# Kernel optimization log

Hardware: AMD Instinct MI355X
Metric: run time of the kernel (lower is better)

## Reference

```python
import jax, jax.numpy as jnp
import numpy as np

N_QUBITS = 4
N_LAYERS = 3
N_FEATURES = 64
BATCH = 524288


def setup_inputs() -> dict:
    key = jax.random.key(0)
    k1, k2, k3, k4 = jax.random.split(key, 4)
    x = jax.random.normal(k1, (BATCH, N_FEATURES), jnp.float32)
    # nn.Linear(64, 4) params
    lim = 1.0 / np.sqrt(N_FEATURES)
    W_pre = jax.random.uniform(k2, (N_QUBITS, N_FEATURES), jnp.float32, -lim, lim)
    b_pre = jax.random.uniform(k3, (N_QUBITS,), jnp.float32, -lim, lim)
    # quantum circuit weights: randn * 0.1
    qweights = jax.random.normal(k4, (N_LAYERS, N_QUBITS, 2), jnp.float32) * 0.1
    return {"x": x, "W_pre": W_pre, "b_pre": b_pre, "qweights": qweights}


def _coef(theta, n):
    # reshape scalar or [B] angle to broadcast against [B, 2,..,2] (n-1 trailing dims after slicing)
    return jnp.reshape(theta, (-1,) + (1,) * (n - 1))


def _apply_ry(state, wire, theta):
    # RY(t) = [[cos t/2, -sin t/2], [sin t/2, cos t/2]] applied on `wire`
    n = state.ndim - 1
    s = jnp.moveaxis(state, 1 + wire, -1)
    a, b = s[..., 0], s[..., 1]
    c = _coef(jnp.cos(theta / 2), n)
    sn = _coef(jnp.sin(theta / 2), n)
    out = jnp.stack([c * a - sn * b, sn * a + c * b], axis=-1)
    return jnp.moveaxis(out, -1, 1 + wire)


def _apply_rz(state, wire, theta):
    # RZ(t) = diag(e^{-i t/2}, e^{+i t/2})
    n = state.ndim - 1
    s = jnp.moveaxis(state, 1 + wire, -1)
    half = _coef(theta / 2, n)
    out = jnp.stack([jnp.exp(-1j * half) * s[..., 0],
                     jnp.exp(1j * half) * s[..., 1]], axis=-1)
    return jnp.moveaxis(out, -1, 1 + wire)


def _apply_cnot(state, ctrl, tgt):
    s = jnp.moveaxis(state, (1 + ctrl, 1 + tgt), (-2, -1))
    s = jnp.concatenate([s[..., 0:1, :], s[..., 1:2, ::-1]], axis=-2)
    return jnp.moveaxis(s, (-2, -1), (1 + ctrl, 1 + tgt))


def _circuit(angles, qweights):
    # batched 4-qubit statevector simulation; state shape [B, 2,2,2,2] (wire 0 = MSB)
    B, n = angles.shape
    nl = qweights.shape[0]
    state = jnp.zeros((B,) + (2,) * n, jnp.complex64)
    state = state.at[(slice(None),) + (0,) * n].set(1.0)
    for w in range(n):
        state = _apply_ry(state, w, angles[:, w])
    for l in range(nl):
        for w in range(n):
            state = _apply_ry(state, w, qweights[l, w, 0])
            state = _apply_rz(state, w, qweights[l, w, 1])
        for w in range(n):
            state = _apply_cnot(state, w, (w + 1) % n)
    probs = state.real ** 2 + state.imag ** 2  # [B, 2,2,2,2] float32
    exps = []
    for w in range(n):
        marg = jnp.moveaxis(probs, 1 + w, 1).reshape(B, 2, -1).sum(-1)  # [B, 2]
        exps.append(marg[:, 0] - marg[:, 1])  # <Z_w>
    return jnp.stack(exps, axis=1)  # [B, n]


def reference(x, W_pre, b_pre, qweights):
    angles = jnp.tanh(x @ W_pre.T + b_pre)  # [B, n_qubits]
    return _circuit(angles, qweights).astype(jnp.float32)
```

## Files before the change

kernel.cpp:

```cpp
#include <hip/hip_runtime.h>
#include <cmath>

__global__ __launch_bounds__(256) void qprep_kernel(
    const float* __restrict__ qw,
    float* __restrict__ A_out)
{
  __shared__ float sre[16][17];
  __shared__ float sim[16][17];
  __shared__ float M[4][16][16];
  const int tid = threadIdx.x;
  const int col = tid >> 4;
  const int u   = tid & 15;

  sre[col][u] = (u == col) ? 1.0f : 0.0f;
  sim[col][u] = 0.0f;
  __syncthreads();

#pragma unroll
  for (int l = 0; l < 3; ++l) {
#pragma unroll
    for (int w = 0; w < 4; ++w) {
      const int mask = 8 >> w;
      float sh, ch, sh2, ch2;
      __sincosf(0.5f * qw[(l * 4 + w) * 2 + 0], &sh, &ch);
      __sincosf(0.5f * qw[(l * 4 + w) * 2 + 1], &sh2, &ch2);
      const int ua = u & ~mask, ub = u | mask;
      const float ar = sre[col][ua], ai = sim[col][ua];
      const float br = sre[col][ub], bi = sim[col][ub];
      __syncthreads();
      float nr, ni;
      if (u & mask) { nr = sh * ar + ch * br; ni = sh * ai + ch * bi; }
      else          { nr = ch * ar - sh * br; ni = ch * ai - sh * bi; }
      float rr, ri;
      if (u & mask) { rr = ch2 * nr - sh2 * ni; ri = ch2 * ni + sh2 * nr; }
      else          { rr = ch2 * nr + sh2 * ni; ri = ch2 * ni - sh2 * nr; }
      sre[col][u] = rr; sim[col][u] = ri;
      __syncthreads();
    }
    int src = u;
    if (src & 1) src ^= 8;
    if (src & 2) src ^= 1;
    if (src & 4) src ^= 2;
    if (src & 8) src ^= 4;
    const float pr = sre[col][src], pi = sim[col][src];
    __syncthreads();
    sre[col][u] = pr; sim[col][u] = pi;
    __syncthreads();
  }

  for (int idx = tid; idx < 1024; idx += 256) {
    const int w = idx >> 8, s = (idx >> 4) & 15, t = idx & 15;
    const int mask = 8 >> w;
    float acc = 0.0f;
#pragma unroll
    for (int uu = 0; uu < 16; ++uu) {
      const float z = (uu & mask) ? -1.0f : 1.0f;
      acc += z * (sre[s][uu] * sre[t][uu] + sim[s][uu] * sim[t][uu]);
    }
    M[w][s][t] = acc;
  }
  __syncthreads();

  for (int idx = tid; idx < 324; idx += 256) {
    const int w = idx & 3, pq = idx >> 2;
    const int p = pq / 9, q = pq % 9;
    const int i0 = p / 3, i1 = p % 3, i2 = q / 3, i3 = q % 3;
    float acc = 0.0f;
#pragma unroll
    for (int comb = 0; comb < 16; ++comb) {
      int s = 0, t = 0;
      float coef = 0.0625f;
      int j;
      j = (comb >> 3) & 1; s |= j << 3; t |= ((i0 == 2) ? (j ^ 1) : j) << 3; if (i0 == 1 && j) coef = -coef;
      j = (comb >> 2) & 1; s |= j << 2; t |= ((i1 == 2) ? (j ^ 1) : j) << 2; if (i1 == 1 && j) coef = -coef;
      j = (comb >> 1) & 1; s |= j << 1; t |= ((i2 == 2) ? (j ^ 1) : j) << 1; if (i2 == 1 && j) coef = -coef;
      j = comb & 1;        s |= j;      t |= ((i3 == 2) ? (j ^ 1) : j);      if (i3 == 1 && j) coef = -coef;
      acc = fmaf(coef, M[w][s][t], acc);
    }
    A_out[idx] = acc;
  }
}

__global__ __launch_bounds__(256) void qmain_kernel(
    const float* __restrict__ x,
    const float* __restrict__ Wp,
    const float* __restrict__ bp,
    const float* __restrict__ A,
    float* __restrict__ out)
{
  __shared__ float xt[256 * 17];
  const int tid = threadIdx.x;
  const size_t row0 = (size_t)blockIdx.x * 256;

  float a0 = 0.f, a1 = 0.f, a2 = 0.f, a3 = 0.f;
#pragma unroll
  for (int c = 0; c < 4; ++c) {
#pragma unroll
    for (int p = 0; p < 4; ++p) {
      const int row = p * 64 + (tid >> 2);
      const int q4 = (tid & 3) << 2;
      const float4 v = *reinterpret_cast<const float4*>(
          x + (row0 + (size_t)row) * 64 + c * 16 + q4);
      float* d = &xt[row * 17 + q4];
      d[0] = v.x; d[1] = v.y; d[2] = v.z; d[3] = v.w;
    }
    __syncthreads();
#pragma unroll
    for (int f = 0; f < 16; ++f) {
      const float xv = xt[tid * 17 + f];
      const int fg = c * 16 + f;
      a0 = fmaf(xv, Wp[fg], a0);
      a1 = fmaf(xv, Wp[64 + fg], a1);
      a2 = fmaf(xv, Wp[128 + fg], a2);
      a3 = fmaf(xv, Wp[192 + fg], a3);
    }
    __syncthreads();
  }

  const float t0 = tanhf(a0 + bp[0]);
  const float t1 = tanhf(a1 + bp[1]);
  const float t2 = tanhf(a2 + bp[2]);
  const float t3 = tanhf(a3 + bp[3]);

  float c0, s0, c1, s1, c2, s2, c3, s3;
  __sincosf(t0, &s0, &c0);
  __sincosf(t1, &s1, &c1);
  __sincosf(t2, &s2, &c2);
  __sincosf(t3, &s3, &c3);

  const float g[9] = {1.f, c1, s1, c0, c0 * c1, c0 * s1, s0, s0 * c1, s0 * s1};
  const float h[9] = {1.f, c3, s3, c2, c2 * c3, c2 * s3, s2, s2 * c3, s2 * s3};

  float e0 = 0.f, e1 = 0.f, e2 = 0.f, e3 = 0.f;
#pragma unroll
  for (int p = 0; p < 9; ++p) {
#pragma unroll
    for (int q = 0; q < 9; ++q) {
      const float t = g[p] * h[q];
      const float* a4 = &A[(p * 9 + q) * 4];
      e0 = fmaf(a4[0], t, e0);
      e1 = fmaf(a4[1], t, e1);
      e2 = fmaf(a4[2], t, e2);
      e3 = fmaf(a4[3], t, e3);
    }
  }
  reinterpret_cast<float4*>(out)[row0 + tid] = make_float4(e0, e1, e2, e3);
}

extern "C" void kernel_launch(void* const* d_in, const int* in_sizes, int n_in,
                              void* d_out, int out_size, void* d_ws, size_t ws_size,
                              hipStream_t stream) {
  const float* x  = (const float*)d_in[0];
  const float* Wp = (const float*)d_in[1];
  const float* bp = (const float*)d_in[2];
  const float* qw = (const float*)d_in[3];
  float* out = (float*)d_out;
  float* A = (float*)d_ws;

  qprep_kernel<<<1, 256, 0, stream>>>(qw, A);

  const int B = in_sizes[0] / 64;
  qmain_kernel<<<B / 256, 256, 0, stream>>>(x, Wp, bp, A, out);
}
```

Baseline: 42.59 us.

## Fuse circuit precompute into main kernel with register-prefetched x loads

Removes the separate single-block prep kernel and has every block recompute the 324-entry coefficient table in LDS. The first x tile is issued into registers before that prep work so the global loads overlap it, and later tiles are prefetched one step ahead. It also swaps tanhf for an __expf-based formula. The cost is redundant per-block prep work, with its many barriers and sincos calls, repeated across 2048 blocks, plus extra register pressure.

```diff
diff --git a/kernel.cpp b/kernel.cpp
--- a/kernel.cpp
+++ b/kernel.cpp
@@ -1,108 +1,122 @@
 #include <hip/hip_runtime.h>
 #include <cmath>
 
-__global__ __launch_bounds__(256) void qprep_kernel(
+__global__ __launch_bounds__(256) void qfused_kernel(
+    const float* __restrict__ x,
+    const float* __restrict__ Wp,
+    const float* __restrict__ bp,
     const float* __restrict__ qw,
-    float* __restrict__ A_out)
+    float* __restrict__ out)
 {
-  __shared__ float sre[16][17];
-  __shared__ float sim[16][17];
-  __shared__ float M[4][16][16];
+  __shared__ float lds[4352 + 324];
+  constexpr int SRE = 0;
+  constexpr int SIM = 272;
+  constexpr int MOF = 544;
+  constexpr int AOF = 4352;
+  float* xt = lds;
+
   const int tid = threadIdx.x;
-  const int col = tid >> 4;
-  const int u   = tid & 15;
+  const size_t row0 = (size_t)blockIdx.x * 256;
 
-  sre[col][u] = (u == col) ? 1.0f : 0.0f;
-  sim[col][u] = 0.0f;
-  __syncthreads();
+  float4 rbuf[4];
+  {
+    const int rrow = tid >> 2, q4 = (tid & 3) << 2;
+#pragma unroll
+    for (int p = 0; p < 4; ++p)
+      rbuf[p] = *reinterpret_cast<const float4*>(
+          x + (row0 + (size_t)(p * 64 + rrow)) * 64 + 0 * 16 + q4);
+  }
+
+  {
+    const int col = tid >> 4;
+    const int u   = tid & 15;
+    lds[SRE + col * 17 + u] = (u == col) ? 1.0f : 0.0f;
+    lds[SIM + col * 17 + u] = 0.0f;
+    __syncthreads();
 
 #pragma unroll
-  for (int l = 0; l < 3; ++l) {
+    for (int l = 0; l < 3; ++l) {
 #pragma unroll
-    for (int w = 0; w < 4; ++w) {
-      const int mask = 8 >> w;
-      float sh, ch, sh2, ch2;
-      __sincosf(0.5f * qw[(l * 4 + w) * 2 + 0], &sh, &ch);
-      __sincosf(0.5f * qw[(l * 4 + w) * 2 + 1], &sh2, &ch2);
-      const int ua = u & ~mask, ub = u | mask;
-      const float ar = sre[col][ua], ai = sim[col][ua];
-      const float br = sre[col][ub], bi = sim[col][ub];
+      for (int w = 0; w < 4; ++w) {
+        const int mask = 8 >> w;
+        float sh, ch, sh2, ch2;
+        __sincosf(0.5f * qw[(l * 4 + w) * 2 + 0], &sh, &ch);
+        __sincosf(0.5f * qw[(l * 4 + w) * 2 + 1], &sh2, &ch2);
+        const int ua = u & ~mask, ub = u | mask;
+        const float ar = lds[SRE + col * 17 + ua], ai = lds[SIM + col * 17 + ua];
+        const float br = lds[SRE + col * 17 + ub], bi = lds[SIM + col * 17 + ub];
+        __syncthreads();
+        float nr, ni;
+        if (u & mask) { nr = sh * ar + ch * br; ni = sh * ai + ch * bi; }
+        else          { nr = ch * ar - sh * br; ni = ch * ai - sh * bi; }
+        float rr, ri;
+        if (u & mask) { rr = ch2 * nr - sh2 * ni; ri = ch2 * ni + sh2 * nr; }
+        else          { rr = ch2 * nr + sh2 * ni; ri = ch2 * ni - sh2 * nr; }
+        lds[SRE + col * 17 + u] = rr; lds[SIM + col * 17 + u] = ri;
+        __syncthreads();
+      }
+      int src = u;
+      if (src & 1) src ^= 8;
+      if (src & 2) src ^= 1;
+      if (src & 4) src ^= 2;
+      if (src & 8) src ^= 4;
+      const float pr = lds[SRE + col * 17 + src], pi = lds[SIM + col * 17 + src];
       __syncthreads();
-      float nr, ni;
-      if (u & mask) { nr = sh * ar + ch * br; ni = sh * ai + ch * bi; }
-      else          { nr = ch * ar - sh * br; ni = ch * ai - sh * bi; }
-      float rr, ri;
-      if (u & mask) { rr = ch2 * nr - sh2 * ni; ri = ch2 * ni + sh2 * nr; }
-      else          { rr = ch2 * nr + sh2 * ni; ri = ch2 * ni - sh2 * nr; }
-      sre[col][u] = rr; sim[col][u] = ri;
+      lds[SRE + col * 17 + u] = pr; lds[SIM + col * 17 + u] = pi;
       __syncthreads();
     }
-    int src = u;
-    if (src & 1) src ^= 8;
-    if (src & 2) src ^= 1;
-    if (src & 4) src ^= 2;
-    if (src & 8) src ^= 4;
-    const float pr = sre[col][src], pi = sim[col][src];
+
+#pragma unroll
+    for (int k = 0; k < 4; ++k) {
+      const int idx = tid + 256 * k;
+      const int w = idx >> 8, s = (idx >> 4) & 15, t = idx & 15;
+      const int mask = 8 >> w;
+      float acc = 0.0f;
+#pragma unroll
+      for (int uu = 0; uu < 16; ++uu) {
+        const float z = (uu & mask) ? -1.0f : 1.0f;
+        acc += z * (lds[SRE + s * 17 + uu] * lds[SRE + t * 17 + uu] +
+                    lds[SIM + s * 17 + uu] * lds[SIM + t * 17 + uu]);
+      }
+      lds[MOF + ((w * 16 + s) * 16 + t)] = acc;
+    }
     __syncthreads();
-    sre[col][u] = pr; sim[col][u] = pi;
+
+    for (int idx = tid; idx < 324; idx += 256) {
+      const int w = idx & 3, pq = idx >> 2;
+      const int p = pq / 9, q = pq % 9;
+      const int i0 = p / 3, i1 = p % 3, i2 = q / 3, i3 = q % 3;
+      float acc = 0.0f;
+#pragma unroll
+      for (int comb = 0; comb < 16; ++comb) {
+        int s = 0, t = 0;
+        float coef = 0.0625f;
+        int j;
+        j = (comb >> 3) & 1; s |= j << 3; t |= ((i0 == 2) ? (j ^ 1) : j) << 3; if (i0 == 1 && j) coef = -coef;
+        j = (comb >> 2) & 1; s |= j << 2; t |= ((i1 == 2) ? (j ^ 1) : j) << 2; if (i1 == 1 && j) coef = -coef;
+        j = (comb >> 1) & 1; s |= j << 1; t |= ((i2 == 2) ? (j ^ 1) : j) << 1; if (i2 == 1 && j) coef = -coef;
+        j = comb & 1;        s |= j;      t |= ((i3 == 2) ? (j ^ 1) : j);      if (i3 == 1 && j) coef = -coef;
+        acc = fmaf(coef, lds[MOF + ((w * 16 + s) * 16 + t)], acc);
+      }
+      lds[AOF + idx] = acc;
+    }
     __syncthreads();
   }
 
-  for (int idx = tid; idx < 1024; idx += 256) {
-    const int w = idx >> 8, s = (idx >> 4) & 15, t = idx & 15;
-    const int mask = 8 >> w;
-    float acc = 0.0f;
-#pragma unroll
-    for (int uu = 0; uu < 16; ++uu) {
-      const float z = (uu & mask) ? -1.0f : 1.0f;
-      acc += z * (sre[s][uu] * sre[t][uu] + sim[s][uu] * sim[t][uu]);
-    }
-    M[w][s][t] = acc;
-  }
-  __syncthreads();
-
-  for (int idx = tid; idx < 324; idx += 256) {
-    const int w = idx & 3, pq = idx >> 2;
-    const int p = pq / 9, q = pq % 9;
-    const int i0 = p / 3, i1 = p % 3, i2 = q / 3, i3 = q % 3;
-    float acc = 0.0f;
-#pragma unroll
-    for (int comb = 0; comb < 16; ++comb) {
-      int s = 0, t = 0;
-      float coef = 0.0625f;
-      int j;
-      j = (comb >> 3) & 1; s |= j << 3; t |= ((i0 == 2) ? (j ^ 1) : j) << 3; if (i0 == 1 && j) coef = -coef;
-      j = (comb >> 2) & 1; s |= j << 2; t |= ((i1 == 2) ? (j ^ 1) : j) << 2; if (i1 == 1 && j) coef = -coef;
-      j = (comb >> 1) & 1; s |= j << 1; t |= ((i2 == 2) ? (j ^ 1) : j) << 1; if (i2 == 1 && j) coef = -coef;
-      j = comb & 1;        s |= j;      t |= ((i3 == 2) ? (j ^ 1) : j);      if (i3 == 1 && j) coef = -coef;
-      acc = fmaf(coef, M[w][s][t], acc);
-    }
-    A_out[idx] = acc;
-  }
-}
-
-__global__ __launch_bounds__(256) void qmain_kernel(
-    const float* __restrict__ x,
-    const float* __restrict__ Wp,
-    const float* __restrict__ bp,
-    const float* __restrict__ A,
-    float* __restrict__ out)
-{
-  __shared__ float xt[256 * 17];
-  const int tid = threadIdx.x;
-  const size_t row0 = (size_t)blockIdx.x * 256;
-
+  const int rrow = tid >> 2, q4 = (tid & 3) << 2;
   float a0 = 0.f, a1 = 0.f, a2 = 0.f, a3 = 0.f;
 #pragma unroll
   for (int c = 0; c < 4; ++c) {
 #pragma unroll
     for (int p = 0; p < 4; ++p) {
-      const int row = p * 64 + (tid >> 2);
-      const int q4 = (tid & 3) << 2;
-      const float4 v = *reinterpret_cast<const float4*>(
-          x + (row0 + (size_t)row) * 64 + c * 16 + q4);
-      float* d = &xt[row * 17 + q4];
-      d[0] = v.x; d[1] = v.y; d[2] = v.z; d[3] = v.w;
+      float* d = &xt[(p * 64 + rrow) * 17 + q4];
+      d[0] = rbuf[p].x; d[1] = rbuf[p].y; d[2] = rbuf[p].z; d[3] = rbuf[p].w;
+    }
+    if (c < 3) {
+#pragma unroll
+      for (int p = 0; p < 4; ++p)
+        rbuf[p] = *reinterpret_cast<const float4*>(
+            x + (row0 + (size_t)(p * 64 + rrow)) * 64 + (c + 1) * 16 + q4);
     }
     __syncthreads();
 #pragma unroll
@@ -114,13 +128,13 @@
       a2 = fmaf(xv, Wp[128 + fg], a2);
       a3 = fmaf(xv, Wp[192 + fg], a3);
     }
-    __syncthreads();
+    if (c < 3) __syncthreads();
   }
 
-  const float t0 = tanhf(a0 + bp[0]);
-  const float t1 = tanhf(a1 + bp[1]);
-  const float t2 = tanhf(a2 + bp[2]);
-  const float t3 = tanhf(a3 + bp[3]);
+  const float t0 = 1.0f - 2.0f / (__expf(2.0f * (a0 + bp[0])) + 1.0f);
+  const float t1 = 1.0f - 2.0f / (__expf(2.0f * (a1 + bp[1])) + 1.0f);
+  const float t2 = 1.0f - 2.0f / (__expf(2.0f * (a2 + bp[2])) + 1.0f);
+  const float t3 = 1.0f - 2.0f / (__expf(2.0f * (a3 + bp[3])) + 1.0f);
 
   float c0, s0, c1, s1, c2, s2, c3, s3;
   __sincosf(t0, &s0, &c0);
@@ -137,11 +151,11 @@
 #pragma unroll
     for (int q = 0; q < 9; ++q) {
       const float t = g[p] * h[q];
-      const float* a4 = &A[(p * 9 + q) * 4];
-      e0 = fmaf(a4[0], t, e0);
-      e1 = fmaf(a4[1], t, e1);
-      e2 = fmaf(a4[2], t, e2);
-      e3 = fmaf(a4[3], t, e3);
+      const int base = AOF + (p * 9 + q) * 4;
+      e0 = fmaf(lds[base + 0], t, e0);
+      e1 = fmaf(lds[base + 1], t, e1);
+      e2 = fmaf(lds[base + 2], t, e2);
+      e3 = fmaf(lds[base + 3], t, e3);
     }
   }
   reinterpret_cast<float4*>(out)[row0 + tid] = make_float4(e0, e1, e2, e3);
@@ -155,10 +169,7 @@
   const float* bp = (const float*)d_in[2];
   const float* qw = (const float*)d_in[3];
   float* out = (float*)d_out;
-  float* A = (float*)d_ws;
-
-  qprep_kernel<<<1, 256, 0, stream>>>(qw, A);
 
   const int B = in_sizes[0] / 64;
-  qmain_kernel<<<B / 256, 256, 0, stream>>>(x, Wp, bp, A, out);
+  qfused_kernel<<<B / 256, 256, 0, stream>>>(x, Wp, bp, qw, out);
 }
```

After: 41.70 us. 1.02x faster.

## Software-pipeline x loads through registers and process two row tiles per block

Applied to the files above, without the earlier changes.

The main kernel now handles 512 rows per block. It double-buffers global loads of x in registers so the next chunk is in flight while the current chunk is staged to LDS and reduced, using lighter custom barriers. LDS stores and reads are vectorised as float4 with a padded stride of 20, tanh is replaced by an exp-based formula, and the A coefficients are read as float4 and shared across two rows. It also pins waves-per-EU to 4. The aim is to hide HBM latency on a bandwidth-bound 128 MB read, at the cost of more registers per thread and half as many blocks.

```diff
diff --git a/kernel.cpp b/kernel.cpp
--- a/kernel.cpp
+++ b/kernel.cpp
@@ -1,5 +1,36 @@
 #include <hip/hip_runtime.h>
 #include <cmath>
+
+
+#define BAR() asm volatile("s_waitcnt lgkmcnt(0)\n\ts_barrier" ::: "memory")
+
+#define LOADX(R0, R1, R2, R3, P, C)                       \
+  R0 = xb[((P) * 256 + 0 * 64) * 16 + (C) * 4];           \
+  R1 = xb[((P) * 256 + 1 * 64) * 16 + (C) * 4];           \
+  R2 = xb[((P) * 256 + 2 * 64) * 16 + (C) * 4];           \
+  R3 = xb[((P) * 256 + 3 * 64) * 16 + (C) * 4];
+
+#define STAGE(R0, R1, R2, R3)                                            \
+  *reinterpret_cast<float4*>(&lds[(0 * 64 + rrow) * XS + q4w]) = R0;     \
+  *reinterpret_cast<float4*>(&lds[(1 * 64 + rrow) * XS + q4w]) = R1;     \
+  *reinterpret_cast<float4*>(&lds[(2 * 64 + rrow) * XS + q4w]) = R2;     \
+  *reinterpret_cast<float4*>(&lds[(3 * 64 + rrow) * XS + q4w]) = R3;
+
+#define GEMV(A0, A1, A2, A3, C) {                                          \
+  const float4 xv0 = *reinterpret_cast<const float4*>(&lds[tid * XS + 0]); \
+  const float4 xv1 = *reinterpret_cast<const float4*>(&lds[tid * XS + 4]); \
+  const float4 xv2 = *reinterpret_cast<const float4*>(&lds[tid * XS + 8]); \
+  const float4 xv3 = *reinterpret_cast<const float4*>(&lds[tid * XS + 12]);\
+  const float xr[16] = {xv0.x, xv0.y, xv0.z, xv0.w, xv1.x, xv1.y, xv1.z,   \
+                        xv1.w, xv2.x, xv2.y, xv2.z, xv2.w, xv3.x, xv3.y,   \
+                        xv3.z, xv3.w};                                     \
+  _Pragma("unroll")                                                        \
+  for (int f = 0; f < 16; ++f) {                                          \
+    A0 = fmaf(xr[f], Wp[(C) * 16 + f], A0);                                \
+    A1 = fmaf(xr[f], Wp[64 + (C) * 16 + f], A1);                           \
+    A2 = fmaf(xr[f], Wp[128 + (C) * 16 + f], A2);                          \
+    A3 = fmaf(xr[f], Wp[192 + (C) * 16 + f], A3);                          \
+  } }
 
 __global__ __launch_bounds__(256) void qprep_kernel(
     const float* __restrict__ qw,
@@ -57,7 +88,7 @@
       const float z = (uu & mask) ? -1.0f : 1.0f;
       acc += z * (sre[s][uu] * sre[t][uu] + sim[s][uu] * sim[t][uu]);
     }
-    M[w][s][t] = acc;
+    M[w >> 0][s][t] = acc;
   }
   __syncthreads();
 
@@ -81,70 +112,95 @@
   }
 }
 
-__global__ __launch_bounds__(256) void qmain_kernel(
+__global__ __launch_bounds__(256)
+__attribute__((amdgpu_waves_per_eu(4, 4)))
+void qmain_kernel(
     const float* __restrict__ x,
     const float* __restrict__ Wp,
     const float* __restrict__ bp,
-    const float* __restrict__ A,
+    const float4* __restrict__ Aws,
     float* __restrict__ out)
 {
-  __shared__ float xt[256 * 17];
+  constexpr int XS = 20;
+  __shared__ alignas(16) float lds[256 * XS];
+
   const int tid = threadIdx.x;
-  const size_t row0 = (size_t)blockIdx.x * 256;
-
-  float a0 = 0.f, a1 = 0.f, a2 = 0.f, a3 = 0.f;
-#pragma unroll
-  for (int c = 0; c < 4; ++c) {
-#pragma unroll
-    for (int p = 0; p < 4; ++p) {
-      const int row = p * 64 + (tid >> 2);
-      const int q4 = (tid & 3) << 2;
-      const float4 v = *reinterpret_cast<const float4*>(
-          x + (row0 + (size_t)row) * 64 + c * 16 + q4);
-      float* d = &xt[row * 17 + q4];
-      d[0] = v.x; d[1] = v.y; d[2] = v.z; d[3] = v.w;
-    }
-    __syncthreads();
-#pragma unroll
-    for (int f = 0; f < 16; ++f) {
-      const float xv = xt[tid * 17 + f];
-      const int fg = c * 16 + f;
-      a0 = fmaf(xv, Wp[fg], a0);
-      a1 = fmaf(xv, Wp[64 + fg], a1);
-      a2 = fmaf(xv, Wp[128 + fg], a2);
-      a3 = fmaf(xv, Wp[192 + fg], a3);
-    }
-    __syncthreads();
-  }
-
-  const float t0 = tanhf(a0 + bp[0]);
-  const float t1 = tanhf(a1 + bp[1]);
-  const float t2 = tanhf(a2 + bp[2]);
-  const float t3 = tanhf(a3 + bp[3]);
-
-  float c0, s0, c1, s1, c2, s2, c3, s3;
-  __sincosf(t0, &s0, &c0);
-  __sincosf(t1, &s1, &c1);
-  __sincosf(t2, &s2, &c2);
-  __sincosf(t3, &s3, &c3);
-
-  const float g[9] = {1.f, c1, s1, c0, c0 * c1, c0 * s1, s0, s0 * c1, s0 * s1};
-  const float h[9] = {1.f, c3, s3, c2, c2 * c3, c2 * s3, s2, s2 * c3, s2 * s3};
-
-  float e0 = 0.f, e1 = 0.f, e2 = 0.f, e3 = 0.f;
+  const size_t row0 = (size_t)blockIdx.x * 512;
+  const int rrow = tid >> 2;
+  const int q4w  = (tid & 3) << 2;
+  const float4* xb = reinterpret_cast<const float4*>(x) +
+                     (row0 + (size_t)rrow) * 16 + (tid & 3);
+
+  float4 rbA0, rbA1, rbA2, rbA3, rbB0, rbB1, rbB2, rbB3;
+  LOADX(rbA0, rbA1, rbA2, rbA3, 0, 0);
+  LOADX(rbB0, rbB1, rbB2, rbB3, 0, 1);
+
+  float aA0 = 0.f, aA1 = 0.f, aA2 = 0.f, aA3 = 0.f;
+  float aB0 = 0.f, aB1 = 0.f, aB2 = 0.f, aB3 = 0.f;
+
+  STAGE(rbA0, rbA1, rbA2, rbA3); LOADX(rbA0, rbA1, rbA2, rbA3, 0, 2); BAR();
+  GEMV(aA0, aA1, aA2, aA3, 0);   BAR();
+  STAGE(rbB0, rbB1, rbB2, rbB3); LOADX(rbB0, rbB1, rbB2, rbB3, 0, 3); BAR();
+  GEMV(aA0, aA1, aA2, aA3, 1);   BAR();
+  STAGE(rbA0, rbA1, rbA2, rbA3); LOADX(rbA0, rbA1, rbA2, rbA3, 1, 0); BAR();
+  GEMV(aA0, aA1, aA2, aA3, 2);   BAR();
+  STAGE(rbB0, rbB1, rbB2, rbB3); LOADX(rbB0, rbB1, rbB2, rbB3, 1, 1); BAR();
+  GEMV(aA0, aA1, aA2, aA3, 3);   BAR();
+  STAGE(rbA0, rbA1, rbA2, rbA3); LOADX(rbA0, rbA1, rbA2, rbA3, 1, 2); BAR();
+  GEMV(aB0, aB1, aB2, aB3, 0);   BAR();
+  STAGE(rbB0, rbB1, rbB2, rbB3); LOADX(rbB0, rbB1, rbB2, rbB3, 1, 3); BAR();
+  GEMV(aB0, aB1, aB2, aB3, 1);   BAR();
+  STAGE(rbA0, rbA1, rbA2, rbA3); BAR();
+  GEMV(aB0, aB1, aB2, aB3, 2);   BAR();
+  STAGE(rbB0, rbB1, rbB2, rbB3); BAR();
+  GEMV(aB0, aB1, aB2, aB3, 3);
+
+  float g0[9], h0[9], g1[9], h1[9];
+  {
+    const float t0 = 1.0f - 2.0f / (__expf(2.0f * (aA0 + bp[0])) + 1.0f);
+    const float t1 = 1.0f - 2.0f / (__expf(2.0f * (aA1 + bp[1])) + 1.0f);
+    const float t2 = 1.0f - 2.0f / (__expf(2.0f * (aA2 + bp[2])) + 1.0f);
+    const float t3 = 1.0f - 2.0f / (__expf(2.0f * (aA3 + bp[3])) + 1.0f);
+    float c0, s0, c1, s1, c2, s2, c3, s3;
+    __sincosf(t0, &s0, &c0); __sincosf(t1, &s1, &c1);
+    __sincosf(t2, &s2, &c2); __sincosf(t3, &s3, &c3);
+    g0[0] = 1.f; g0[1] = c1; g0[2] = s1; g0[3] = c0; g0[4] = c0 * c1;
+    g0[5] = c0 * s1; g0[6] = s0; g0[7] = s0 * c1; g0[8] = s0 * s1;
+    h0[0] = 1.f; h0[1] = c3; h0[2] = s3; h0[3] = c2; h0[4] = c2 * c3;
+    h0[5] = c2 * s3; h0[6] = s2; h0[7] = s2 * c3; h0[8] = s2 * s3;
+  }
+  {
+    const float t0 = 1.0f - 2.0f / (__expf(2.0f * (aB0 + bp[0])) + 1.0f);
+    const float t1 = 1.0f - 2.0f / (__expf(2.0f * (aB1 + bp[1])) + 1.0f);
+    const float t2 = 1.0f - 2.0f / (__expf(2.0f * (aB2 + bp[2])) + 1.0f);
+    const float t3 = 1.0f - 2.0f / (__expf(2.0f * (aB3 + bp[3])) + 1.0f);
+    float c0, s0, c1, s1, c2, s2, c3, s3;
+    __sincosf(t0, &s0, &c0); __sincosf(t1, &s1, &c1);
+    __sincosf(t2, &s2, &c2); __sincosf(t3, &s3, &c3);
+    g1[0] = 1.f; g1[1] = c1; g1[2] = s1; g1[3] = c0; g1[4] = c0 * c1;
+    g1[5] = c0 * s1; g1[6] = s0; g1[7] = s0 * c1; g1[8] = s0 * s1;
+    h1[0] = 1.f; h1[1] = c3; h1[2] = s3; h1[3] = c2; h1[4] = c2 * c3;
+    h1[5] = c2 * s3; h1[6] = s2; h1[7] = s2 * c3; h1[8] = s2 * s3;
+  }
+
+  float e00 = 0.f, e01 = 0.f, e02 = 0.f, e03 = 0.f;
+  float e10 = 0.f, e11 = 0.f, e12 = 0.f, e13 = 0.f;
 #pragma unroll
   for (int p = 0; p < 9; ++p) {
 #pragma unroll
     for (int q = 0; q < 9; ++q) {
-      const float t = g[p] * h[q];
-      const float* a4 = &A[(p * 9 + q) * 4];
-      e0 = fmaf(a4[0], t, e0);
-      e1 = fmaf(a4[1], t, e1);
-      e2 = fmaf(a4[2], t, e2);
-      e3 = fmaf(a4[3], t, e3);
-    }
-  }
-  reinterpret_cast<float4*>(out)[row0 + tid] = make_float4(e0, e1, e2, e3);
+      const float4 a4 = Aws[p * 9 + q];
+      const float tA = g0[p] * h0[q];
+      const float tB = g1[p] * h1[q];
+      e00 = fmaf(a4.x, tA, e00); e01 = fmaf(a4.y, tA, e01);
+      e02 = fmaf(a4.z, tA, e02); e03 = fmaf(a4.w, tA, e03);
+      e10 = fmaf(a4.x, tB, e10); e11 = fmaf(a4.y, tB, e11);
+      e12 = fmaf(a4.z, tB, e12); e13 = fmaf(a4.w, tB, e13);
+    }
+  }
+  float4* out4 = reinterpret_cast<float4*>(out);
+  out4[row0 + tid]       = make_float4(e00, e01, e02, e03);
+  out4[row0 + 256 + tid] = make_float4(e10, e11, e12, e13);
 }
 
 extern "C" void kernel_launch(void* const* d_in, const int* in_sizes, int n_in,
@@ -156,9 +212,11 @@
   const float* qw = (const float*)d_in[3];
   float* out = (float*)d_out;
   float* A = (float*)d_ws;
+  (void)n_in; (void)out_size; (void)ws_size;
 
   qprep_kernel<<<1, 256, 0, stream>>>(qw, A);
 
   const int B = in_sizes[0] / 64;
-  qmain_kernel<<<B / 256, 256, 0, stream>>>(x, Wp, bp, A, out);
+  qmain_kernel<<<B / 512, 256, 0, stream>>>(x, Wp, bp,
+                                            (const float4*)A, out);
 }
```

Result: faster. 38.27 us (-10.1%).

## Restructure main kernel to single-wave blocks with register-prefetched x tiles

Applied to the files above, without the earlier changes.

The main kernel now uses a single 64-thread wave per block, with each block processing 256 rows as four 64-row tiles. The next tile's x data is prefetched into registers while the current tile is transposed through padded LDS and reduced. Block-wide barriers are dropped in favour of an explicit lgkmcnt wait, and the waves-per-EU attribute is pinned. tanhf is replaced by an exp-based formula, which adds rounding error and relies on the single wave being its own synchronisation scope.

```diff
diff --git a/kernel.cpp b/kernel.cpp
--- a/kernel.cpp
+++ b/kernel.cpp
@@ -1,5 +1,6 @@
 #include <hip/hip_runtime.h>
 #include <cmath>
+
 
 __global__ __launch_bounds__(256) void qprep_kernel(
     const float* __restrict__ qw,
@@ -81,70 +82,100 @@
   }
 }
 
-__global__ __launch_bounds__(256) void qmain_kernel(
+__global__ __launch_bounds__(64)
+__attribute__((amdgpu_waves_per_eu(2, 2)))
+void qmain_kernel(
     const float* __restrict__ x,
     const float* __restrict__ Wp,
     const float* __restrict__ bp,
-    const float* __restrict__ A,
+    const float4* __restrict__ Aws,
     float* __restrict__ out)
 {
-  __shared__ float xt[256 * 17];
-  const int tid = threadIdx.x;
-  const size_t row0 = (size_t)blockIdx.x * 256;
+  constexpr int RS = 68;
+  __shared__ alignas(16) float wlds[64 * RS];
 
-  float a0 = 0.f, a1 = 0.f, a2 = 0.f, a3 = 0.f;
+  const int lane = threadIdx.x;
+  const int hi   = lane >> 4;
+  const int c4   = (lane & 15) << 2;
+  const size_t wrow0 = (size_t)blockIdx.x * 256;
+
+  const float4* xs  = reinterpret_cast<const float4*>(x);
+  float4* out4      = reinterpret_cast<float4*>(out);
+
+  float4 v[16];
+  {
+    const float4* src = xs + wrow0 * 16 + lane;
 #pragma unroll
-  for (int c = 0; c < 4; ++c) {
-#pragma unroll
-    for (int p = 0; p < 4; ++p) {
-      const int row = p * 64 + (tid >> 2);
-      const int q4 = (tid & 3) << 2;
-      const float4 v = *reinterpret_cast<const float4*>(
-          x + (row0 + (size_t)row) * 64 + c * 16 + q4);
-      float* d = &xt[row * 17 + q4];
-      d[0] = v.x; d[1] = v.y; d[2] = v.z; d[3] = v.w;
-    }
-    __syncthreads();
-#pragma unroll
-    for (int f = 0; f < 16; ++f) {
-      const float xv = xt[tid * 17 + f];
-      const int fg = c * 16 + f;
-      a0 = fmaf(xv, Wp[fg], a0);
-      a1 = fmaf(xv, Wp[64 + fg], a1);
-      a2 = fmaf(xv, Wp[128 + fg], a2);
-      a3 = fmaf(xv, Wp[192 + fg], a3);
-    }
-    __syncthreads();
+    for (int i = 0; i < 16; ++i) v[i] = src[i * 64];
   }
 
-  const float t0 = tanhf(a0 + bp[0]);
-  const float t1 = tanhf(a1 + bp[1]);
-  const float t2 = tanhf(a2 + bp[2]);
-  const float t3 = tanhf(a3 + bp[3]);
+#pragma unroll
+  for (int t = 0; t < 4; ++t) {
+    const size_t r0 = wrow0 + (size_t)(t * 64);
 
-  float c0, s0, c1, s1, c2, s2, c3, s3;
-  __sincosf(t0, &s0, &c0);
-  __sincosf(t1, &s1, &c1);
-  __sincosf(t2, &s2, &c2);
-  __sincosf(t3, &s3, &c3);
+#pragma unroll
+    for (int i = 0; i < 16; ++i)
+      *reinterpret_cast<float4*>(&wlds[(4 * i + hi) * RS + c4]) = v[i];
 
-  const float g[9] = {1.f, c1, s1, c0, c0 * c1, c0 * s1, s0, s0 * c1, s0 * s1};
-  const float h[9] = {1.f, c3, s3, c2, c2 * c3, c2 * s3, s2, s2 * c3, s2 * s3};
+    if (t < 3) {
+      const float4* src = xs + (r0 + 64) * 16 + lane;
+#pragma unroll
+      for (int i = 0; i < 16; ++i) v[i] = src[i * 64];
+    }
 
-  float e0 = 0.f, e1 = 0.f, e2 = 0.f, e3 = 0.f;
+    asm volatile("s_waitcnt lgkmcnt(0)" ::: "memory");
+    __builtin_amdgcn_sched_barrier(0);
+
+    float a0 = 0.f, a1 = 0.f, a2 = 0.f, a3 = 0.f;
 #pragma unroll
-  for (int p = 0; p < 9; ++p) {
+    for (int j = 0; j < 16; ++j) {
+      const float4 q =
+          *reinterpret_cast<const float4*>(&wlds[lane * RS + j * 4]);
+      a0 = fmaf(q.x, Wp[j * 4 + 0], a0);
+      a0 = fmaf(q.y, Wp[j * 4 + 1], a0);
+      a0 = fmaf(q.z, Wp[j * 4 + 2], a0);
+      a0 = fmaf(q.w, Wp[j * 4 + 3], a0);
+      a1 = fmaf(q.x, Wp[64 + j * 4 + 0], a1);
+      a1 = fmaf(q.y, Wp[64 + j * 4 + 1], a1);
+      a1 = fmaf(q.z, Wp[64 + j * 4 + 2], a1);
+      a1 = fmaf(q.w, Wp[64 + j * 4 + 3], a1);
+      a2 = fmaf(q.x, Wp[128 + j * 4 + 0], a2);
+      a2 = fmaf(q.y, Wp[128 + j * 4 + 1], a2);
+      a2 = fmaf(q.z, Wp[128 + j * 4 + 2], a2);
+      a2 = fmaf(q.w, Wp[128 + j * 4 + 3], a2);
+      a3 = fmaf(q.x, Wp[192 + j * 4 + 0], a3);
+      a3 = fmaf(q.y, Wp[192 + j * 4 + 1], a3);
+      a3 = fmaf(q.z, Wp[192 + j * 4 + 2], a3);
+      a3 = fmaf(q.w, Wp[192 + j * 4 + 3], a3);
+    }
+
+    const float t0 = 1.0f - 2.0f / (__expf(2.0f * (a0 + bp[0])) + 1.0f);
+    const float t1 = 1.0f - 2.0f / (__expf(2.0f * (a1 + bp[1])) + 1.0f);
+    const float t2 = 1.0f - 2.0f / (__expf(2.0f * (a2 + bp[2])) + 1.0f);
+    const float t3 = 1.0f - 2.0f / (__expf(2.0f * (a3 + bp[3])) + 1.0f);
+
+    float c0, s0, c1, s1, c2, s2, c3, s3;
+    __sincosf(t0, &s0, &c0); __sincosf(t1, &s1, &c1);
+    __sincosf(t2, &s2, &c2); __sincosf(t3, &s3, &c3);
+
+    const float g[9] = {1.f, c1, s1, c0, c0 * c1, c0 * s1,
+                        s0, s0 * c1, s0 * s1};
+    const float h[9] = {1.f, c3, s3, c2, c2 * c3, c2 * s3,
+                        s2, s2 * c3, s2 * s3};
+
+    float e0 = 0.f, e1 = 0.f, e2 = 0.f, e3 = 0.f;
 #pragma unroll
-    for (int q = 0; q < 9; ++q) {
-      const float t = g[p] * h[q];
-      const float* a4 = &A[(p * 9 + q) * 4];
-      e0 = fmaf(a4[0], t, e0);
-      e1 = fmaf(a4[1], t, e1);
-      e2 = fmaf(a4[2], t, e2);
-      e3 = fmaf(a4[3], t, e3);
+    for (int p = 0; p < 9; ++p) {
+#pragma unroll
+      for (int q2 = 0; q2 < 9; ++q2) {
+        const float4 a4 = Aws[p * 9 + q2];
+        const float tt = g[p] * h[q2];
+        e0 = fmaf(a4.x, tt, e0); e1 = fmaf(a4.y, tt, e1);
+        e2 = fmaf(a4.z, tt, e2); e3 = fmaf(a4.w, tt, e3);
+      }
     }
+    out4[r0 + lane] = make_float4(e0, e1, e2, e3);
   }
-  reinterpret_cast<float4*>(out)[row0 + tid] = make_float4(e0, e1, e2, e3);
 }
 
 extern "C" void kernel_launch(void* const* d_in, const int* in_sizes, int n_in,
@@ -156,9 +187,11 @@
   const float* qw = (const float*)d_in[3];
   float* out = (float*)d_out;
   float* A = (float*)d_ws;
+  (void)n_in; (void)out_size; (void)ws_size;
 
   qprep_kernel<<<1, 256, 0, stream>>>(qw, A);
 
   const int B = in_sizes[0] / 64;
-  qmain_kernel<<<B / 256, 256, 0, stream>>>(x, Wp, bp, A, out);
+  qmain_kernel<<<B / 256, 64, 0, stream>>>(x, Wp, bp,
+                                           (const float4*)A, out);
 }
```

After: 68.72 us. +61.3%, slower.
